# Performance work log

Hardware: AMD Instinct MI355X
Metric: run time of the kernel (lower is better)

The kernel has to match this reference:

```python
import jax, jax.numpy as jnp
import numpy as np

N = 262144          # number of query points
NUM_AXES = 4        # input_dim + 2
RES = 512           # axis_resolution
EMB = 256           # embedding_dim
OUT = 3             # output_dim
W0 = 30.0           # Sine frequency


def setup_inputs() -> dict:
    key = jax.random.key(0)
    k_c, k_t, k_w1, k_b1, k_w2, k_b2 = jax.random.split(key, 6)
    coords = jax.random.uniform(k_c, (N, 2), jnp.float32, minval=-1.0, maxval=1.0)
    tables = jax.random.normal(k_t, (NUM_AXES, RES, EMB), jnp.float32) * 0.1
    # decoder: Linear(256,256) with first_layer_sine_init, Sine(30), Linear(256,3) with frequency_init(30)
    W1 = jax.random.uniform(k_w1, (256, EMB), jnp.float32, minval=-1.0 / EMB, maxval=1.0 / EMB)
    b1 = jax.random.uniform(k_b1, (256,), jnp.float32, minval=-0.0625, maxval=0.0625)
    lim2 = np.sqrt(6.0 / 256.0) / W0
    W2 = jax.random.uniform(k_w2, (OUT, 256), jnp.float32, minval=-lim2, maxval=lim2)
    b2 = jax.random.uniform(k_b2, (OUT,), jnp.float32, minval=-0.0625, maxval=0.0625)
    return {"coords": coords, "tables": tables, "W1": W1, "b1": b1, "W2": W2, "b2": b2}


def reference(coords, tables, W1, b1, W2, b2):
    # clamp input coords to [-1,1], build the 4 axis coordinates
    c = jnp.clip(coords, -1.0, 1.0)
    c = jnp.concatenate(
        [c, (c[:, 0:1] + c[:, 1:2]) * 0.5, (c[:, 0:1] - c[:, 1:2]) * 0.5], axis=-1
    )  # [N, 4]
    # linearInterpolate (vectorized over all axes at once)
    c = jnp.clip(c, -1.0, 0.999)
    t = (0.5 * c + 0.5) * (tables.shape[1] - 1)       # [N, 4] continuous index
    i0 = jnp.floor(t).astype(jnp.int32)               # [N, 4]
    w = (t - i0)[..., None]                           # [N, 4, 1]
    ax = jnp.arange(tables.shape[0])[None, :]         # [1, 4]
    v0 = tables[ax, i0]                               # [N, 4, EMB] gather
    v1 = tables[ax, i0 + 1]                           # [N, 4, EMB] gather
    emb = jnp.mean((1.0 - w) * v0 + w * v1, axis=1)   # [N, EMB] mean over axes
    # decoder: Linear -> Sine(30) -> Linear
    h = jnp.sin(W0 * (emb @ W1.T + b1))               # [N, 256]
    return h @ W2.T + b2                              # [N, 3]
```

## Files before the change

kernel.cpp:

```cpp
#include <hip/hip_runtime.h>
#include <hip/hip_fp16.h>

#define NPTS 262144
#define EMB  256
#define NROWS 2048

typedef _Float16 half_t;
typedef __attribute__((ext_vector_type(8))) _Float16 half8;
typedef __attribute__((ext_vector_type(2))) _Float16 half2v;

__global__ __launch_bounds__(256) void t2_precompute_kernel(
    const float* __restrict__ tables,
    const float* __restrict__ W1,
    half_t* __restrict__ T2)
{
    __shared__ __align__(16) float arow[8][EMB];
    const int row0 = blockIdx.x * 8;
    const int o = threadIdx.x;

    #pragma unroll
    for (int r = 0; r < 8; ++r)
        arow[r][o] = tables[(row0 + r) * EMB + o];
    __syncthreads();

    float acc[8] = {0.f, 0.f, 0.f, 0.f, 0.f, 0.f, 0.f, 0.f};
    const float4* __restrict__ w1v = reinterpret_cast<const float4*>(W1 + o * EMB);
    for (int ec = 0; ec < EMB / 4; ++ec) {
        const float4 w4 = w1v[ec];
        #pragma unroll
        for (int r = 0; r < 8; ++r) {
            const float4 a4 = *reinterpret_cast<const float4*>(&arow[r][ec * 4]);
            acc[r] = fmaf(w4.x, a4.x, acc[r]);
            acc[r] = fmaf(w4.y, a4.y, acc[r]);
            acc[r] = fmaf(w4.z, a4.z, acc[r]);
            acc[r] = fmaf(w4.w, a4.w, acc[r]);
        }
    }
    const float s = 7.5f * 0.15915494309189535f;
    #pragma unroll
    for (int r = 0; r < 8; ++r)
        T2[(row0 + r) * EMB + o] = (half_t)(s * acc[r]);
}

template <int CTRL>
__device__ __forceinline__ float dpp_add(float v) {
    const int vi = __builtin_bit_cast(int, v);
    const int sh = __builtin_amdgcn_update_dpp(0, vi, CTRL, 0xF, 0xF, true);
    return v + __builtin_bit_cast(float, sh);
}
__device__ __forceinline__ float reduce16(float v) {
    v = dpp_add<0xB1>(v);
    v = dpp_add<0x4E>(v);
    v = dpp_add<0x141>(v);
    v = dpp_add<0x140>(v);
    return v;
}

__global__ __launch_bounds__(256, 4) void eval_kernel(
    const float* __restrict__ coords,
    const half_t* __restrict__ T2,
    const float* __restrict__ b1,
    const float* __restrict__ W2,
    const float* __restrict__ b2,
    float* __restrict__ out)
{
    const int lane = threadIdx.x & 63;
    const int g    = lane >> 4;
    const int l16  = lane & 15;
    const int dA   = l16 * 8;
    const int dB   = 128 + l16 * 8;

    const int wave   = blockIdx.x * 4 + (threadIdx.x >> 6);
    const int stride = gridDim.x * 4;

    const float sb = 30.f * 0.15915494309189535f;
    half8 biasA, biasB;
    #pragma unroll
    for (int i = 0; i < 8; ++i) {
        biasA[i] = (half_t)(sb * b1[dA + i]);
        biasB[i] = (half_t)(sb * b1[dB + i]);
    }
    half2v w2A[3][4], w2B[3][4];
    #pragma unroll
    for (int j = 0; j < 3; ++j)
        #pragma unroll
        for (int k = 0; k < 4; ++k) {
            w2A[j][k][0] = (half_t)W2[j * EMB + dA + 2 * k];
            w2A[j][k][1] = (half_t)W2[j * EMB + dA + 2 * k + 1];
            w2B[j][k][0] = (half_t)W2[j * EMB + dB + 2 * k];
            w2B[j][k][1] = (half_t)W2[j * EMB + dB + 2 * k + 1];
        }
    const float ob0 = b2[0], ob1 = b2[1], ob2 = b2[2];

    int Ca[4];
    #pragma unroll
    for (int a = 0; a < 4; ++a) Ca[a] = (a << 18) + (l16 << 4);

    const char* __restrict__ T2b = reinterpret_cast<const char*>(T2);
    const float TMAX = 0.9995f * 511.0f;

    auto calc = [&](int pq, int rb[4], half2v pw[4], int& pOut) {
        const int p = 4 * pq + g;
        pOut = p;
        const float2 cf = *reinterpret_cast<const float2*>(coords + 2 * p);
        const float txr = __builtin_amdgcn_fmed3f(fmaf(cf.x, 255.5f, 255.5f), 0.f, 511.f);
        const float tyr = __builtin_amdgcn_fmed3f(fmaf(cf.y, 255.5f, 255.5f), 0.f, 511.f);
        float t[4];
        t[0] = fminf(txr, TMAX);
        t[1] = fminf(tyr, TMAX);
        t[2] = fminf((txr + tyr) * 0.5f, TMAX);
        t[3] = fminf(fmaf(txr - tyr, 0.5f, 255.5f), TMAX);
        #pragma unroll
        for (int a = 0; a < 4; ++a) {
            const int i0 = (int)t[a];
            const float w = t[a] - (float)i0;
            rb[a] = (i0 << 9) + Ca[a];
            pw[a] = __builtin_bit_cast(half2v,
                        __builtin_amdgcn_cvt_pkrtz(1.f - w, w));
        }
    };
    auto loadA = [&](const int rb[4], half8 A0[4], half8 A1[4]) {
        #pragma unroll
        for (int a = 0; a < 4; ++a) {
            A0[a] = *reinterpret_cast<const half8*>(T2b + rb[a]);
            A1[a] = *reinterpret_cast<const half8*>(T2b + rb[a] + 512);
        }
    };
    auto loadB = [&](const int rb[4], half8 B0[4], half8 B1[4]) {
        #pragma unroll
        for (int a = 0; a < 4; ++a) {
            B0[a] = *reinterpret_cast<const half8*>(T2b + rb[a] + 256);
            B1[a] = *reinterpret_cast<const half8*>(T2b + rb[a] + 768);
        }
    };
    auto dots = [&](const half8& acc, const half2v (&w2)[3][4],
                    float& q0, float& q1, float& q2) {
        #pragma unroll
        for (int k = 0; k < 4; ++k) {
            const float s0 = __builtin_amdgcn_sinf((float)acc[2 * k]);
            const float s1 = __builtin_amdgcn_sinf((float)acc[2 * k + 1]);
            const half2v hp = __builtin_bit_cast(half2v,
                                  __builtin_amdgcn_cvt_pkrtz(s0, s1));
            q0 = __builtin_amdgcn_fdot2(hp, w2[0][k], q0, false);
            q1 = __builtin_amdgcn_fdot2(hp, w2[1][k], q1, false);
            q2 = __builtin_amdgcn_fdot2(hp, w2[2][k], q2, false);
        }
    };

    int    rbC[4]; half2v pwC[4]; int pC;
    int    rbN[4]; half2v pwN[4]; int pN = 0;
    half8  A0[4], A1[4], B0[4], B1[4];

    calc(wave, rbC, pwC, pC);
    loadA(rbC, A0, A1);
    loadB(rbC, B0, B1);

    #pragma unroll
    for (int k = 0; k < 8; ++k) {
        if (k < 7) calc(wave + (k + 1) * stride, rbN, pwN, pN);

        half8 accA = biasA;
        #pragma unroll
        for (int a = 0; a < 4; ++a) {
            accA = A0[a] * pwC[a][0] + accA;
            accA = A1[a] * pwC[a][1] + accA;
        }
        if (k < 7) loadA(rbN, A0, A1);

        float q0 = 0.f, q1 = 0.f, q2 = 0.f;
        dots(accA, w2A, q0, q1, q2);

        half8 accB = biasB;
        #pragma unroll
        for (int a = 0; a < 4; ++a) {
            accB = B0[a] * pwC[a][0] + accB;
            accB = B1[a] * pwC[a][1] + accB;
        }
        if (k < 7) loadB(rbN, B0, B1);

        dots(accB, w2B, q0, q1, q2);

        q0 = reduce16(q0);
        q1 = reduce16(q1);
        q2 = reduce16(q2);

        if (l16 == 0) {
            *reinterpret_cast<float3*>(out + 3 * pC) =
                make_float3(q0 + ob0, q1 + ob1, q2 + ob2);
        }

        #pragma unroll
        for (int a = 0; a < 4; ++a) { rbC[a] = rbN[a]; pwC[a] = pwN[a]; }
        pC = pN;
    }
}

extern "C" void kernel_launch(void* const* d_in, const int* in_sizes, int n_in,
                              void* d_out, int out_size, void* d_ws, size_t ws_size,
                              hipStream_t stream) {
    const float* coords = (const float*)d_in[0];
    const float* tables = (const float*)d_in[1];
    const float* W1     = (const float*)d_in[2];
    const float* b1     = (const float*)d_in[3];
    const float* W2     = (const float*)d_in[4];
    const float* b2     = (const float*)d_in[5];
    float* out = (float*)d_out;

    half_t* T2 = (half_t*)d_ws;

    hipLaunchKernelGGL(t2_precompute_kernel, dim3(NROWS / 8), dim3(256), 0, stream,
                       tables, W1, T2);
    hipLaunchKernelGGL(eval_kernel, dim3(2048), dim3(256), 0, stream,
                       coords, T2, b1, W2, b2, out);
}
```

Before: 55.32 us.

## Store precomputed table-projection in FP8 and interpolate in fp32 with double-buffered loads

The precomputed table×W1 product is now stored as FP8 (scaled by 64) instead of fp16, which halves the bytes gathered per query point. The eval kernel decodes FP8 to fp32, interpolates in fp32, then rescales and adds the bias before the sine. It also double-buffers the next point's loads and handles 16 contiguous channels per lane, with launch bounds lowered to 3 blocks per SM. The risks are accuracy loss from FP8 quantisation before a high-frequency sine, extra conversion ALU work, and lower occupancy.

```diff
diff --git a/kernel.cpp b/kernel.cpp
--- a/kernel.cpp
+++ b/kernel.cpp
@@ -6,15 +6,15 @@
 #define NROWS 2048
 
 typedef _Float16 half_t;
-typedef __attribute__((ext_vector_type(8))) _Float16 half8;
 typedef __attribute__((ext_vector_type(2))) _Float16 half2v;
 
-__global__ __launch_bounds__(256) void t2_precompute_kernel(
+__global__ __launch_bounds__(256) void t8_precompute_kernel(
     const float* __restrict__ tables,
     const float* __restrict__ W1,
-    half_t* __restrict__ T2)
+    unsigned int* __restrict__ T8)
 {
     __shared__ __align__(16) float arow[8][EMB];
+    __shared__ __align__(16) float prow[8][EMB];
     const int row0 = blockIdx.x * 8;
     const int o = threadIdx.x;
 
@@ -36,10 +36,22 @@
             acc[r] = fmaf(w4.w, a4.w, acc[r]);
         }
     }
-    const float s = 7.5f * 0.15915494309189535f;
+    const float s = 64.f * 7.5f * 0.15915494309189535f;
     #pragma unroll
     for (int r = 0; r < 8; ++r)
-        T2[(row0 + r) * EMB + o] = (half_t)(s * acc[r]);
+        prow[r][o] = s * acc[r];
+    __syncthreads();
+
+    #pragma unroll
+    for (int hh = 0; hh < 2; ++hh) {
+        const int gidx = o + hh * 256;
+        const int r    = gidx >> 6;
+        const int dw   = gidx & 63;
+        const float* p = &prow[r][dw * 4];
+        int v = __builtin_amdgcn_cvt_pk_fp8_f32(p[0], p[1], 0, false);
+        v     = __builtin_amdgcn_cvt_pk_fp8_f32(p[2], p[3], v, true);
+        T8[(row0 + r) * 64 + dw] = (unsigned int)v;
+    }
 }
 
 template <int CTRL>
@@ -56,9 +68,9 @@
     return v;
 }
 
-__global__ __launch_bounds__(256, 4) void eval_kernel(
+__global__ __launch_bounds__(256, 3) void eval_kernel(
     const float* __restrict__ coords,
-    const half_t* __restrict__ T2,
+    const char* __restrict__ T8b,
     const float* __restrict__ b1,
     const float* __restrict__ W2,
     const float* __restrict__ b2,
@@ -67,41 +79,36 @@
     const int lane = threadIdx.x & 63;
     const int g    = lane >> 4;
     const int l16  = lane & 15;
-    const int dA   = l16 * 8;
-    const int dB   = 128 + l16 * 8;
+    const int d0   = l16 * 16;
 
     const int wave   = blockIdx.x * 4 + (threadIdx.x >> 6);
     const int stride = gridDim.x * 4;
 
-    const float sb = 30.f * 0.15915494309189535f;
-    half8 biasA, biasB;
-    #pragma unroll
-    for (int i = 0; i < 8; ++i) {
-        biasA[i] = (half_t)(sb * b1[dA + i]);
-        biasB[i] = (half_t)(sb * b1[dB + i]);
-    }
-    half2v w2A[3][4], w2B[3][4];
+    const float sb  = 30.f * 0.15915494309189535f;
+    const float c64 = 0.015625f;
+    half_t biash[16];
+    #pragma unroll
+    for (int i = 0; i < 16; ++i) biash[i] = (half_t)(sb * b1[d0 + i]);
+    half2v w2p[3][8];
     #pragma unroll
     for (int j = 0; j < 3; ++j)
         #pragma unroll
-        for (int k = 0; k < 4; ++k) {
-            w2A[j][k][0] = (half_t)W2[j * EMB + dA + 2 * k];
-            w2A[j][k][1] = (half_t)W2[j * EMB + dA + 2 * k + 1];
-            w2B[j][k][0] = (half_t)W2[j * EMB + dB + 2 * k];
-            w2B[j][k][1] = (half_t)W2[j * EMB + dB + 2 * k + 1];
+        for (int k = 0; k < 8; ++k) {
+            w2p[j][k][0] = (half_t)W2[j * EMB + d0 + 2 * k];
+            w2p[j][k][1] = (half_t)W2[j * EMB + d0 + 2 * k + 1];
         }
     const float ob0 = b2[0], ob1 = b2[1], ob2 = b2[2];
-
-    int Ca[4];
-    #pragma unroll
-    for (int a = 0; a < 4; ++a) Ca[a] = (a << 18) + (l16 << 4);
-
-    const char* __restrict__ T2b = reinterpret_cast<const char*>(T2);
+    const int laneoff = l16 << 4;
     const float TMAX = 0.9995f * 511.0f;
 
-    auto calc = [&](int pq, int rb[4], half2v pw[4], int& pOut) {
+    int    rb[2][4];
+    half2v wg[2][4];
+    int    pC[2];
+    uint4  R0[2][4], R1[2][4];
+
+    auto calc = [&](int pq, int s) {
         const int p = 4 * pq + g;
-        pOut = p;
+        pC[s] = p;
         const float2 cf = *reinterpret_cast<const float2*>(coords + 2 * p);
         const float txr = __builtin_amdgcn_fmed3f(fmaf(cf.x, 255.5f, 255.5f), 0.f, 511.f);
         const float tyr = __builtin_amdgcn_fmed3f(fmaf(cf.y, 255.5f, 255.5f), 0.f, 511.f);
@@ -112,86 +119,78 @@
         t[3] = fminf(fmaf(txr - tyr, 0.5f, 255.5f), TMAX);
         #pragma unroll
         for (int a = 0; a < 4; ++a) {
-            const int i0 = (int)t[a];
+            const int i0  = (int)t[a];
             const float w = t[a] - (float)i0;
-            rb[a] = (i0 << 9) + Ca[a];
-            pw[a] = __builtin_bit_cast(half2v,
-                        __builtin_amdgcn_cvt_pkrtz(1.f - w, w));
+            rb[s][a] = (((a << 9) + i0) << 8) + laneoff;
+            wg[s][a] = __builtin_bit_cast(half2v,
+                           __builtin_amdgcn_cvt_pkrtz(1.f - w, w));
         }
     };
-    auto loadA = [&](const int rb[4], half8 A0[4], half8 A1[4]) {
+    auto loads = [&](int s) {
         #pragma unroll
         for (int a = 0; a < 4; ++a) {
-            A0[a] = *reinterpret_cast<const half8*>(T2b + rb[a]);
-            A1[a] = *reinterpret_cast<const half8*>(T2b + rb[a] + 512);
+            R0[s][a] = *reinterpret_cast<const uint4*>(T8b + rb[s][a]);
+            R1[s][a] = *reinterpret_cast<const uint4*>(T8b + rb[s][a] + 256);
         }
     };
-    auto loadB = [&](const int rb[4], half8 B0[4], half8 B1[4]) {
+
+    calc(wave, 0);
+    loads(0);
+
+    #pragma unroll
+    for (int k = 0; k < 8; ++k) {
+        const int s  = k & 1;
+        const int ns = s ^ 1;
+        if (k < 7) { calc(wave + (k + 1) * stride, ns); loads(ns); }
+
+        float acc[16];
+        #pragma unroll
+        for (int i = 0; i < 16; ++i) acc[i] = 0.f;
         #pragma unroll
         for (int a = 0; a < 4; ++a) {
-            B0[a] = *reinterpret_cast<const half8*>(T2b + rb[a] + 256);
-            B1[a] = *reinterpret_cast<const half8*>(T2b + rb[a] + 768);
-        }
-    };
-    auto dots = [&](const half8& acc, const half2v (&w2)[3][4],
-                    float& q0, float& q1, float& q2) {
-        #pragma unroll
-        for (int k = 0; k < 4; ++k) {
-            const float s0 = __builtin_amdgcn_sinf((float)acc[2 * k]);
-            const float s1 = __builtin_amdgcn_sinf((float)acc[2 * k + 1]);
+            const float omw = (float)wg[s][a][0];
+            const float w   = (float)wg[s][a][1];
+            const unsigned int* u0 = reinterpret_cast<const unsigned int*>(&R0[s][a]);
+            const unsigned int* u1 = reinterpret_cast<const unsigned int*>(&R1[s][a]);
+            #pragma unroll
+            for (int q = 0; q < 4; ++q) {
+                auto p0l = __builtin_amdgcn_cvt_pk_f32_fp8(u0[q], false);
+                auto p0h = __builtin_amdgcn_cvt_pk_f32_fp8(u0[q], true);
+                auto p1l = __builtin_amdgcn_cvt_pk_f32_fp8(u1[q], false);
+                auto p1h = __builtin_amdgcn_cvt_pk_f32_fp8(u1[q], true);
+                acc[4*q+0] = fmaf(p0l[0], omw, acc[4*q+0]);
+                acc[4*q+0] = fmaf(p1l[0], w,   acc[4*q+0]);
+                acc[4*q+1] = fmaf(p0l[1], omw, acc[4*q+1]);
+                acc[4*q+1] = fmaf(p1l[1], w,   acc[4*q+1]);
+                acc[4*q+2] = fmaf(p0h[0], omw, acc[4*q+2]);
+                acc[4*q+2] = fmaf(p1h[0], w,   acc[4*q+2]);
+                acc[4*q+3] = fmaf(p0h[1], omw, acc[4*q+3]);
+                acc[4*q+3] = fmaf(p1h[1], w,   acc[4*q+3]);
+            }
+        }
+
+        float q0 = 0.f, q1 = 0.f, q2 = 0.f;
+        #pragma unroll
+        for (int kk = 0; kk < 8; ++kk) {
+            const float a0 = fmaf(acc[2*kk],   c64, (float)biash[2*kk]);
+            const float a1 = fmaf(acc[2*kk+1], c64, (float)biash[2*kk+1]);
+            const float s0 = __builtin_amdgcn_sinf(a0);
+            const float s1 = __builtin_amdgcn_sinf(a1);
             const half2v hp = __builtin_bit_cast(half2v,
                                   __builtin_amdgcn_cvt_pkrtz(s0, s1));
-            q0 = __builtin_amdgcn_fdot2(hp, w2[0][k], q0, false);
-            q1 = __builtin_amdgcn_fdot2(hp, w2[1][k], q1, false);
-            q2 = __builtin_amdgcn_fdot2(hp, w2[2][k], q2, false);
-        }
-    };
-
-    int    rbC[4]; half2v pwC[4]; int pC;
-    int    rbN[4]; half2v pwN[4]; int pN = 0;
-    half8  A0[4], A1[4], B0[4], B1[4];
-
-    calc(wave, rbC, pwC, pC);
-    loadA(rbC, A0, A1);
-    loadB(rbC, B0, B1);
-
-    #pragma unroll
-    for (int k = 0; k < 8; ++k) {
-        if (k < 7) calc(wave + (k + 1) * stride, rbN, pwN, pN);
-
-        half8 accA = biasA;
-        #pragma unroll
-        for (int a = 0; a < 4; ++a) {
-            accA = A0[a] * pwC[a][0] + accA;
-            accA = A1[a] * pwC[a][1] + accA;
-        }
-        if (k < 7) loadA(rbN, A0, A1);
-
-        float q0 = 0.f, q1 = 0.f, q2 = 0.f;
-        dots(accA, w2A, q0, q1, q2);
-
-        half8 accB = biasB;
-        #pragma unroll
-        for (int a = 0; a < 4; ++a) {
-            accB = B0[a] * pwC[a][0] + accB;
-            accB = B1[a] * pwC[a][1] + accB;
-        }
-        if (k < 7) loadB(rbN, B0, B1);
-
-        dots(accB, w2B, q0, q1, q2);
+            q0 = __builtin_amdgcn_fdot2(hp, w2p[0][kk], q0, false);
+            q1 = __builtin_amdgcn_fdot2(hp, w2p[1][kk], q1, false);
+            q2 = __builtin_amdgcn_fdot2(hp, w2p[2][kk], q2, false);
+        }
 
         q0 = reduce16(q0);
         q1 = reduce16(q1);
         q2 = reduce16(q2);
 
         if (l16 == 0) {
-            *reinterpret_cast<float3*>(out + 3 * pC) =
+            *reinterpret_cast<float3*>(out + 3 * pC[s]) =
                 make_float3(q0 + ob0, q1 + ob1, q2 + ob2);
         }
-
-        #pragma unroll
-        for (int a = 0; a < 4; ++a) { rbC[a] = rbN[a]; pwC[a] = pwN[a]; }
-        pC = pN;
     }
 }
 
@@ -206,10 +205,10 @@
     const float* b2     = (const float*)d_in[5];
     float* out = (float*)d_out;
 
-    half_t* T2 = (half_t*)d_ws;
-
-    hipLaunchKernelGGL(t2_precompute_kernel, dim3(NROWS / 8), dim3(256), 0, stream,
-                       tables, W1, T2);
+    unsigned int* T8 = (unsigned int*)d_ws;
+
+    hipLaunchKernelGGL(t8_precompute_kernel, dim3(NROWS / 8), dim3(256), 0, stream,
+                       tables, W1, T8);
     hipLaunchKernelGGL(eval_kernel, dim3(2048), dim3(256), 0, stream,
-                       coords, T2, b1, W2, b2, out);
-}
+                       coords, (const char*)T8, b1, W2, b2, out);
+}
```

New measurement: 58.77 us. 6.2% more time.
